# Kernel tuning notes

Measured on AMD Instinct MI355X. Metric: run time of the kernel, lower is better.

The kernel has to match this reference:

```python
import jax, jax.numpy as jnp
import numpy as np

EPS = 1e-5

def _layernorm(x, g, b):
    mu = jnp.mean(x, axis=-1, keepdims=True)
    var = jnp.var(x, axis=-1, keepdims=True)
    return (x - mu) * jax.lax.rsqrt(var + EPS) * g + b

def _pos_encoding(S, D, dtype):
    pos = jnp.arange(S, dtype=jnp.float32)[:, None]
    div = jnp.exp(jnp.arange(0, D, 2, dtype=jnp.float32) * (-jnp.log(10000.0) / D))
    pe = jnp.zeros((S, D), dtype=jnp.float32)
    pe = pe.at[:, 0::2].set(jnp.sin(pos * div))
    pe = pe.at[:, 1::2].set(jnp.cos(pos * div))
    return pe.astype(dtype)

def setup_inputs() -> dict:
    key = jax.random.key(0)
    B, S, D, H, F, L = 4, 1024, 768, 12, 3072, 6
    ks = jax.random.split(key, 8)
    s = 0.02
    return {
        "x": jax.random.normal(ks[0], (B, S, D), jnp.float32),
        "Wqkv": jax.random.normal(ks[1], (L, D, 3 * D), jnp.float32) * s,
        "bqkv": jnp.zeros((L, 3 * D), jnp.float32),
        "Wo": jax.random.normal(ks[2], (L, D, D), jnp.float32) * s,
        "bo": jnp.zeros((L, D), jnp.float32),
        "ln1_g": jnp.ones((L, D), jnp.float32),
        "ln1_b": jnp.zeros((L, D), jnp.float32),
        "W1": jax.random.normal(ks[3], (L, D, F), jnp.float32) * s,
        "b1": jnp.zeros((L, F), jnp.float32),
        "W2": jax.random.normal(ks[4], (L, F, D), jnp.float32) * s,
        "b2": jnp.zeros((L, D), jnp.float32),
        "ln2_g": jnp.ones((L, D), jnp.float32),
        "ln2_b": jnp.zeros((L, D), jnp.float32),
        "lnf_g": jnp.ones((D,), jnp.float32),
        "lnf_b": jnp.zeros((D,), jnp.float32),
        "num_heads": 12,
    }

def reference(x, Wqkv, bqkv, Wo, bo, ln1_g, ln1_b, W1, b1, W2, b2, ln2_g, ln2_b, lnf_g, lnf_b, num_heads):
    B, S, D = x.shape
    H = num_heads
    hd = D // H
    scale = 1.0 / jnp.sqrt(jnp.float32(hd)).astype(x.dtype)

    x = x + _pos_encoding(S, D, x.dtype)[None]

    def layer(h, params):
        wqkv, bq, wo, bo_, g1, b1_, w1, bias1, w2, bias2, g2, b2_ = params
        qkv = (h @ wqkv + bq).reshape(B, S, 3, H, hd)
        q, k, v = jnp.moveaxis(qkv, 2, 0)          # each [B,S,H,hd]
        q = q.transpose(0, 2, 1, 3)                 # bhqd
        k = k.transpose(0, 2, 1, 3)
        v = v.transpose(0, 2, 1, 3)
        scores = jnp.einsum('bhqd,bhkd->bhqk', q, k) * scale
        w = jax.nn.softmax(scores, axis=-1)
        w = jnp.clip(w, 1e-6, 1.0)                  # clamp as in torch module
        attn = jnp.einsum('bhqk,bhkd->bhqd', w, v)
        attn = attn.transpose(0, 2, 1, 3).reshape(B, S, D) @ wo + bo_
        h = _layernorm(h + attn, g1, b1_)
        ffn = jax.nn.relu(h @ w1 + bias1) @ w2 + bias2
        h = _layernorm(h + ffn, g2, b2_)
        return h, None

    params = (Wqkv, bqkv, Wo, bo, ln1_g, ln1_b, W1, b1, W2, b2, ln2_g, ln2_b)
    x, _ = jax.lax.scan(layer, x, params)
    return _layernorm(x, lnf_g, lnf_b)
```

## Files before the change

kernel.cpp:

```cpp
#include <hip/hip_runtime.h>
#include <math.h>

typedef float f32x4 __attribute__((ext_vector_type(4)));
typedef __bf16 bf16x8 __attribute__((ext_vector_type(8)));
typedef unsigned short u16x8 __attribute__((ext_vector_type(8)));

__device__ __forceinline__ unsigned short f2bf(float f) {
    union { float f; unsigned int u; } v; v.f = f;
    unsigned int r = v.u + 0x7FFFu + ((v.u >> 16) & 1u);
    return (unsigned short)(r >> 16);
}
__device__ __forceinline__ float bf2f(unsigned short u) {
    union { unsigned int u; float f; } v; v.u = ((unsigned int)u) << 16;
    return v.f;
}
__device__ __forceinline__ bf16x8 ld8(const unsigned short* p) {
    union { u16x8 u; bf16x8 b; } c;
    c.u = *(const u16x8*)p;
    return c.b;
}
__device__ __forceinline__ void gload_lds16(const unsigned short* g, unsigned short* l) {
    __builtin_amdgcn_global_load_lds(
        (const __attribute__((address_space(1))) unsigned int*)g,
        (__attribute__((address_space(3))) unsigned int*)l,
        16, 0, 0);
}
__device__ __forceinline__ int swz_off(int row, int quad) {
    return row * 32 + ((quad ^ ((row >> 1) & 3)) << 3);
}

__global__ __launch_bounds__(256)
void transpose_convert(const float* __restrict__ W, unsigned short* __restrict__ Wt,
                       int K, int N) {
    __shared__ float tile[32][33];
    int n0 = blockIdx.x * 32, k0 = blockIdx.y * 32;
    int tx = threadIdx.x & 31, ty = threadIdx.x >> 5;
#pragma unroll
    for (int i = 0; i < 4; ++i) {
        int k = ty + i * 8;
        tile[k][tx] = W[(size_t)(k0 + k) * N + n0 + tx];
    }
    __syncthreads();
#pragma unroll
    for (int i = 0; i < 4; ++i) {
        int n = ty + i * 8;
        Wt[(size_t)(n0 + n) * K + k0 + tx] = f2bf(tile[tx][n]);
    }
}

__global__ __launch_bounds__(256)
void posenc_k(const float* __restrict__ x, float* __restrict__ h,
              unsigned short* __restrict__ hb) {
    int idx = blockIdx.x * 256 + threadIdx.x;
    const int TOT = 4 * 1024 * 768;
    if (idx >= TOT) return;
    int d = idx % 768;
    int s = (idx / 768) % 1024;
    int i2 = d >> 1;
    float dv = expf(-(float)(2 * i2) * (9.210340371976184f / 768.0f));
    float ang = (float)s * dv;
    float pe = (d & 1) ? cosf(ang) : sinf(ang);
    float v = x[idx] + pe;
    h[idx] = v;
    hb[idx] = f2bf(v);
}

template<int RELU, int BIAS>
__global__ __launch_bounds__(256)
void gemm_k(const unsigned short* __restrict__ A, const unsigned short* __restrict__ Bt,
            const float* __restrict__ bias, unsigned short* __restrict__ Cb,
            int M, int N, int K, int Kc) {
    __shared__ unsigned short As[2][128 * 32];
    __shared__ unsigned short Bs[2][128 * 32];
    const int tid = threadIdx.x;
    const int lane = tid & 63, wave = tid >> 6;
    const int l15 = lane & 15, quad = lane >> 4;
    const int m0 = blockIdx.y * 128, n0 = blockIdx.x * 128;
    const int wr = (wave >> 1) * 64, wc = (wave & 1) * 64;
    const int kstart = blockIdx.z * Kc;
    unsigned short* Cbp = Cb + (size_t)blockIdx.z * M * N;

    const int r0 = wave * 32 + (lane >> 2);
    const int kc0 = lane & 3;

    auto stage = [&](int k0, int bi) {
#pragma unroll
        for (int j = 0; j < 2; ++j) {
            int r = r0 + j * 16;
            int kcl = kc0 ^ ((r >> 1) & 3);
            gload_lds16(A + (size_t)(m0 + r) * K + k0 + kcl * 8,
                        &As[bi][(wave * 32 + j * 16) * 32]);
            gload_lds16(Bt + (size_t)(n0 + r) * K + k0 + kcl * 8,
                        &Bs[bi][(wave * 32 + j * 16) * 32]);
        }
    };

    f32x4 acc[4][4];
#pragma unroll
    for (int i = 0; i < 4; ++i)
#pragma unroll
        for (int j = 0; j < 4; ++j) acc[i][j] = (f32x4){0.f, 0.f, 0.f, 0.f};

    stage(kstart, 0);
    const int nk = Kc / 32;
    for (int t = 0; t < nk; ++t) {
        __syncthreads();
        if (t + 1 < nk) stage(kstart + (t + 1) * 32, (t + 1) & 1);
        const unsigned short* Asb = As[t & 1];
        const unsigned short* Bsb = Bs[t & 1];
        bf16x8 af[4], bfr[4];
#pragma unroll
        for (int mt = 0; mt < 4; ++mt)
            af[mt] = ld8(&Asb[swz_off(wr + mt * 16 + l15, quad)]);
#pragma unroll
        for (int nt = 0; nt < 4; ++nt)
            bfr[nt] = ld8(&Bsb[swz_off(wc + nt * 16 + l15, quad)]);
#pragma unroll
        for (int mt = 0; mt < 4; ++mt)
#pragma unroll
            for (int nt = 0; nt < 4; ++nt)
                acc[mt][nt] = __builtin_amdgcn_mfma_f32_16x16x32_bf16(
                    af[mt], bfr[nt], acc[mt][nt], 0, 0, 0);
    }
#pragma unroll
    for (int mt = 0; mt < 4; ++mt)
#pragma unroll
        for (int nt = 0; nt < 4; ++nt)
#pragma unroll
            for (int r = 0; r < 4; ++r) {
                int row = m0 + wr + mt * 16 + quad * 4 + r;
                int col = n0 + wc + nt * 16 + l15;
                float v = acc[mt][nt][r];
                if (BIAS) v += bias[col];
                if (RELU) v = fmaxf(v, 0.f);
                Cbp[(size_t)row * N + col] = f2bf(v);
            }
}

__global__ __launch_bounds__(256)
void qksplit_k(const unsigned short* __restrict__ qkv, unsigned short* __restrict__ Q,
               unsigned short* __restrict__ Ko) {
    int o8 = blockIdx.x * 256 + threadIdx.x;
    const int NQ8 = 393216;
    int which = (o8 >= NQ8) ? 1 : 0;
    int oo = o8 - which * NQ8;
    int dg = (oo & 7) * 8;
    int s = (oo >> 3) & 1023;
    int bh = oo >> 13;
    int h = bh % 12, b = bh / 12;
    size_t row = (size_t)(b * 1024 + s);
    int col = which * 768 + h * 64 + dg;
    u16x8 val = *(const u16x8*)&qkv[row * 2304 + col];
    if (!which) {
#pragma unroll
        for (int j = 0; j < 8; ++j) val[j] = f2bf(bf2f(val[j]) * 0.125f);
        *(u16x8*)&Q[((size_t)bh * 1024 + s) * 64 + dg] = val;
    } else {
        *(u16x8*)&Ko[((size_t)bh * 1024 + s) * 64 + dg] = val;
    }
}

__global__ __launch_bounds__(256)
void vt_k(const unsigned short* __restrict__ qkv, unsigned short* __restrict__ Vt) {
    __shared__ unsigned short t[64][65];
    int bh = blockIdx.y, s0 = blockIdx.x * 64;
    int b = bh / 12, h = bh % 12;
    int tx = threadIdx.x & 63;
    int ty = threadIdx.x >> 6;
#pragma unroll
    for (int r = 0; r < 16; ++r) {
        int i = ty + r * 4;
        t[i][tx] = qkv[(size_t)(b * 1024 + s0 + i) * 2304 + 1536 + h * 64 + tx];
    }
    __syncthreads();
#pragma unroll
    for (int r = 0; r < 16; ++r) {
        int dd = ty + r * 4;
        Vt[((size_t)bh * 64 + dd) * 1024 + s0 + tx] = t[tx][dd];
    }
}

#define PSTR 68
__global__ __launch_bounds__(256)
void flash_k(const unsigned short* __restrict__ Q, const unsigned short* __restrict__ K,
             const unsigned short* __restrict__ Vt, unsigned short* __restrict__ ctx) {
    const int S = 1024, HD = 64;
    int bh = blockIdx.y;
    int b = bh / 12, h = bh % 12;
    int q0 = blockIdx.x * 64;
    const unsigned short* Qp = Q + ((size_t)bh * S + q0) * HD;
    const unsigned short* Kp = K + (size_t)bh * S * HD;
    const unsigned short* Vp = Vt + (size_t)bh * HD * S;

    __shared__ unsigned short Qs[128 * 32];
    __shared__ unsigned short Ks[2][128 * 32];
    __shared__ unsigned short Vs[2][128 * 32];
    __shared__ unsigned short Ps[4 * 16 * PSTR];

    int tid = threadIdx.x;
    int lane = tid & 63, wave = tid >> 6;
    int l15 = lane & 15, quad = lane >> 4;

    const int rl0 = lane >> 2;
    const int c0 = lane & 3;

    auto stageKV = [&](int kt, int bi) {
#pragma unroll
        for (int j = 0; j < 2; ++j) {
            int R = wave * 32 + j * 16 + rl0;
            int khalf = R >> 6, grow = R & 63;
            int lch = c0 ^ ((R >> 1) & 3);
            gload_lds16(Kp + (kt * 64 + grow) * HD + khalf * 32 + lch * 8,
                        &Ks[bi][(wave * 32 + j * 16) * 32]);
            gload_lds16(Vp + (size_t)grow * S + kt * 64 + khalf * 32 + lch * 8,
                        &Vs[bi][(wave * 32 + j * 16) * 32]);
        }
    };

#pragma unroll
    for (int j = 0; j < 2; ++j) {
        int R = wave * 32 + j * 16 + rl0;
        int khalf = R >> 6, grow = R & 63;
        int lch = c0 ^ ((R >> 1) & 3);
        gload_lds16(Qp + grow * HD + khalf * 32 + lch * 8,
                    &Qs[(wave * 32 + j * 16) * 32]);
    }
    stageKV(0, 0);

    f32x4 o[4];
#pragma unroll
    for (int i = 0; i < 4; ++i) o[i] = (f32x4){0.f, 0.f, 0.f, 0.f};
    float lsum[4] = {0.f, 0.f, 0.f, 0.f};

    unsigned short* Pw = &Ps[wave * 16 * PSTR];

    for (int kt = 0; kt < 16; ++kt) {
        __syncthreads();
        if (kt < 15) stageKV(kt + 1, (kt + 1) & 1);
        const unsigned short* Ksb = Ks[kt & 1];
        const unsigned short* Vsb = Vs[kt & 1];

        bf16x8 qa0 = ld8(&Qs[swz_off(wave * 16 + l15, quad)]);
        bf16x8 qa1 = ld8(&Qs[swz_off(64 + wave * 16 + l15, quad)]);
        f32x4 sc[4];
#pragma unroll
        for (int cb = 0; cb < 4; ++cb) {
            bf16x8 kb0 = ld8(&Ksb[swz_off(cb * 16 + l15, quad)]);
            bf16x8 kb1 = ld8(&Ksb[swz_off(64 + cb * 16 + l15, quad)]);
            f32x4 z = (f32x4){0.f, 0.f, 0.f, 0.f};
            z = __builtin_amdgcn_mfma_f32_16x16x32_bf16(qa0, kb0, z, 0, 0, 0);
            z = __builtin_amdgcn_mfma_f32_16x16x32_bf16(qa1, kb1, z, 0, 0, 0);
            sc[cb] = z;
        }
#pragma unroll
        for (int cb = 0; cb < 4; ++cb)
#pragma unroll
            for (int r = 0; r < 4; ++r) {
                float pv = __expf(sc[cb][r]);
                sc[cb][r] = pv;
                lsum[r] += pv;
            }
#pragma unroll
        for (int cb = 0; cb < 4; ++cb)
#pragma unroll
            for (int r = 0; r < 4; ++r)
                Pw[(quad * 4 + r) * PSTR + cb * 16 + l15] = f2bf(sc[cb][r]);
        bf16x8 pa0 = ld8(&Pw[l15 * PSTR + quad * 8]);
        bf16x8 pa1 = ld8(&Pw[l15 * PSTR + 32 + quad * 8]);
#pragma unroll
        for (int cb = 0; cb < 4; ++cb) {
            bf16x8 vb0 = ld8(&Vsb[swz_off(cb * 16 + l15, quad)]);
            bf16x8 vb1 = ld8(&Vsb[swz_off(64 + cb * 16 + l15, quad)]);
            o[cb] = __builtin_amdgcn_mfma_f32_16x16x32_bf16(pa0, vb0, o[cb], 0, 0, 0);
            o[cb] = __builtin_amdgcn_mfma_f32_16x16x32_bf16(pa1, vb1, o[cb], 0, 0, 0);
        }
    }
#pragma unroll
    for (int r = 0; r < 4; ++r) {
#pragma unroll
        for (int off = 1; off < 16; off <<= 1) lsum[r] += __shfl_xor(lsum[r], off);
    }
#pragma unroll
    for (int cb = 0; cb < 4; ++cb)
#pragma unroll
        for (int r = 0; r < 4; ++r) {
            int row = q0 + wave * 16 + quad * 4 + r;
            float val = o[cb][r] / lsum[r];
            ctx[((size_t)(b * 1024 + row)) * 768 + h * 64 + cb * 16 + l15] = f2bf(val);
        }
}

template<int NPART, int WBF16>
__global__ __launch_bounds__(256)
void ln_k(const float* __restrict__ X, const unsigned short* __restrict__ P,
          const float* __restrict__ pb,
          const float* __restrict__ g, const float* __restrict__ bta,
          float* __restrict__ Yf, unsigned short* __restrict__ Yb) {
    const int D = 768;
    const size_t MD = (size_t)4096 * 768;
    int row = blockIdx.x;
    int tid = threadIdx.x;
    const float* x = X + (size_t)row * D;
    float v[3];
    float s = 0.f, s2 = 0.f;
#pragma unroll
    for (int i = 0; i < 3; ++i) {
        int c = i * 256 + tid;
        float t = x[c];
        if (NPART > 0) {
            float r = pb[c];
#pragma unroll
            for (int pi = 0; pi < NPART; ++pi)
                r += bf2f(P[MD * pi + (size_t)row * D + c]);
            t += r;
        }
        v[i] = t;
        s += t;
        s2 += t * t;
    }
#pragma unroll
    for (int off = 1; off < 64; off <<= 1) {
        s += __shfl_xor(s, off);
        s2 += __shfl_xor(s2, off);
    }
    __shared__ float rs[4], rs2[4];
    int wave = tid >> 6, lane = tid & 63;
    if (lane == 0) { rs[wave] = s; rs2[wave] = s2; }
    __syncthreads();
    s = rs[0] + rs[1] + rs[2] + rs[3];
    s2 = rs2[0] + rs2[1] + rs2[2] + rs2[3];
    float mu = s * (1.f / 768.f);
    float var = s2 * (1.f / 768.f) - mu * mu;
    float rstd = rsqrtf(var + 1e-5f);
#pragma unroll
    for (int i = 0; i < 3; ++i) {
        int c = i * 256 + tid;
        float y = (v[i] - mu) * rstd * g[c] + bta[c];
        Yf[(size_t)row * D + c] = y;
        if (WBF16) Yb[(size_t)row * D + c] = f2bf(y);
    }
}

extern "C" void kernel_launch(void* const* d_in, const int* in_sizes, int n_in,
                              void* d_out, int out_size, void* d_ws, size_t ws_size,
                              hipStream_t stream) {
    const float* x    = (const float*)d_in[0];
    const float* Wqkv = (const float*)d_in[1];
    const float* bqkv = (const float*)d_in[2];
    const float* Wo   = (const float*)d_in[3];
    const float* bo   = (const float*)d_in[4];
    const float* ln1g = (const float*)d_in[5];
    const float* ln1b = (const float*)d_in[6];
    const float* W1   = (const float*)d_in[7];
    const float* b1   = (const float*)d_in[8];
    const float* W2   = (const float*)d_in[9];
    const float* b2   = (const float*)d_in[10];
    const float* ln2g = (const float*)d_in[11];
    const float* ln2b = (const float*)d_in[12];
    const float* lnfg = (const float*)d_in[13];
    const float* lnfb = (const float*)d_in[14];

    const int B = 4, S = 1024, D = 768, H = 12, F = 3072, L = 6;
    const int M = B * S;

    char* p = (char*)d_ws;
    auto alloc = [&](size_t bytes) -> char* {
        char* r = p;
        p += (bytes + 255) & ~(size_t)255;
        return r;
    };
    float* h             = (float*)alloc((size_t)M * D * 4);
    unsigned short* tmp  = (unsigned short*)alloc((size_t)4 * M * D * 2);
    unsigned short* hb   = (unsigned short*)alloc((size_t)M * D * 2);
    unsigned short* act  = (unsigned short*)alloc((size_t)M * F * 2);
    unsigned short* Qb   = (unsigned short*)alloc((size_t)M * D * 2);
    unsigned short* Kb   = (unsigned short*)alloc((size_t)M * D * 2);
    unsigned short* Vtb  = (unsigned short*)alloc((size_t)M * D * 2);
    unsigned short* ctx  = (unsigned short*)alloc((size_t)M * D * 2);
    unsigned short* wqkvT = (unsigned short*)alloc((size_t)3 * D * D * 2);
    unsigned short* woT   = (unsigned short*)alloc((size_t)D * D * 2);
    unsigned short* w1T   = (unsigned short*)alloc((size_t)D * F * 2);
    unsigned short* w2T   = (unsigned short*)alloc((size_t)D * F * 2);
    unsigned short* qkvb = act;
    unsigned short* f1b  = act;

    posenc_k<<<(M * D) / 256, 256, 0, stream>>>(x, h, hb);

    for (int l = 0; l < L; ++l) {
        transpose_convert<<<dim3(3 * D / 32, D / 32), 256, 0, stream>>>(
            Wqkv + (size_t)l * D * 3 * D, wqkvT, D, 3 * D);
        transpose_convert<<<dim3(D / 32, D / 32), 256, 0, stream>>>(
            Wo + (size_t)l * D * D, woT, D, D);
        transpose_convert<<<dim3(F / 32, D / 32), 256, 0, stream>>>(
            W1 + (size_t)l * D * F, w1T, D, F);
        transpose_convert<<<dim3(D / 32, F / 32), 256, 0, stream>>>(
            W2 + (size_t)l * F * D, w2T, F, D);

        gemm_k<0, 1><<<dim3(3 * D / 128, M / 128, 1), 256, 0, stream>>>(
            hb, wqkvT, bqkv + (size_t)l * 3 * D, qkvb, M, 3 * D, D, D);
        qksplit_k<<<786432 / 256, 256, 0, stream>>>(qkvb, Qb, Kb);
        vt_k<<<dim3(S / 64, B * H), 256, 0, stream>>>(qkvb, Vtb);
        flash_k<<<dim3(S / 64, B * H), 256, 0, stream>>>(Qb, Kb, Vtb, ctx);
        gemm_k<0, 0><<<dim3(D / 128, M / 128, 4), 256, 0, stream>>>(
            ctx, woT, nullptr, tmp, M, D, D, D / 4);
        ln_k<4, 1><<<M, 256, 0, stream>>>(h, tmp, bo + (size_t)l * D,
                                          ln1g + (size_t)l * D, ln1b + (size_t)l * D,
                                          h, hb);
        gemm_k<1, 1><<<dim3(F / 128, M / 128, 1), 256, 0, stream>>>(
            hb, w1T, b1 + (size_t)l * F, f1b, M, F, D, D);
        gemm_k<0, 0><<<dim3(D / 128, M / 128, 4), 256, 0, stream>>>(
            f1b, w2T, nullptr, tmp, M, D, F, F / 4);
        ln_k<4, 1><<<M, 256, 0, stream>>>(h, tmp, b2 + (size_t)l * D,
                                          ln2g + (size_t)l * D, ln2b + (size_t)l * D,
                                          h, hb);
    }
    ln_k<0, 0><<<M, 256, 0, stream>>>(h, nullptr, nullptr, lnfg, lnfb,
                                      (float*)d_out, nullptr);
}
```

Before: 1.319 ms.

## Split attention over key halves, fuse weight prep and QKV split kernels

Merges the four weight transpose-convert launches into one kernel, and merges the Q/K split and V transpose into one kernel. Q is now prescaled by 0.125·log2(e) so the softmax can use exp2. The flash kernel splits the key range across two z-blocks, single-buffers K/V to cut LDS use, computes row sums with an MFMA against a ones vector, and writes partial outputs that a new combine kernel adds and normalizes. This is meant to raise occupancy and parallelism in attention and reduce launch count. In exchange it costs an extra pass over the partial outputs, drops K/V prefetch overlap, and rounds P by truncation rather than round-to-nearest.

```diff
diff --git a/kernel.cpp b/kernel.cpp
--- a/kernel.cpp
+++ b/kernel.cpp
@@ -9,6 +9,10 @@
     union { float f; unsigned int u; } v; v.f = f;
     unsigned int r = v.u + 0x7FFFu + ((v.u >> 16) & 1u);
     return (unsigned short)(r >> 16);
+}
+__device__ __forceinline__ unsigned short f2bft(float f) {
+    union { float f; unsigned int u; } v; v.f = f;
+    return (unsigned short)(v.u >> 16);
 }
 __device__ __forceinline__ float bf2f(unsigned short u) {
     union { unsigned int u; float f; } v; v.u = ((unsigned int)u) << 16;
@@ -30,10 +34,19 @@
 }
 
 __global__ __launch_bounds__(256)
-void transpose_convert(const float* __restrict__ W, unsigned short* __restrict__ Wt,
-                       int K, int N) {
+void wprep_k(const float* __restrict__ Wqkv, const float* __restrict__ Wo,
+             const float* __restrict__ W1, const float* __restrict__ W2,
+             unsigned short* __restrict__ qkvT, unsigned short* __restrict__ woT,
+             unsigned short* __restrict__ w1T, unsigned short* __restrict__ w2T) {
     __shared__ float tile[32][33];
-    int n0 = blockIdx.x * 32, k0 = blockIdx.y * 32;
+    int bid = blockIdx.x;
+    const float* W; unsigned short* Wt; int K, N, idx;
+    if (bid < 1728)      { W = Wqkv; Wt = qkvT; K = 768;  N = 2304; idx = bid; }
+    else if (bid < 2304) { W = Wo;   Wt = woT;  K = 768;  N = 768;  idx = bid - 1728; }
+    else if (bid < 4608) { W = W1;   Wt = w1T;  K = 768;  N = 3072; idx = bid - 2304; }
+    else                 { W = W2;   Wt = w2T;  K = 3072; N = 768;  idx = bid - 4608; }
+    int ntile = N / 32;
+    int n0 = (idx % ntile) * 32, k0 = (idx / ntile) * 32;
     int tx = threadIdx.x & 31, ty = threadIdx.x >> 5;
 #pragma unroll
     for (int i = 0; i < 4; ++i) {
@@ -138,40 +151,31 @@
 }
 
 __global__ __launch_bounds__(256)
-void qksplit_k(const unsigned short* __restrict__ qkv, unsigned short* __restrict__ Q,
-               unsigned short* __restrict__ Ko) {
-    int o8 = blockIdx.x * 256 + threadIdx.x;
-    const int NQ8 = 393216;
-    int which = (o8 >= NQ8) ? 1 : 0;
-    int oo = o8 - which * NQ8;
-    int dg = (oo & 7) * 8;
-    int s = (oo >> 3) & 1023;
-    int bh = oo >> 13;
-    int h = bh % 12, b = bh / 12;
-    size_t row = (size_t)(b * 1024 + s);
-    int col = which * 768 + h * 64 + dg;
-    u16x8 val = *(const u16x8*)&qkv[row * 2304 + col];
-    if (!which) {
-#pragma unroll
-        for (int j = 0; j < 8; ++j) val[j] = f2bf(bf2f(val[j]) * 0.125f);
-        *(u16x8*)&Q[((size_t)bh * 1024 + s) * 64 + dg] = val;
-    } else {
-        *(u16x8*)&Ko[((size_t)bh * 1024 + s) * 64 + dg] = val;
-    }
-}
-
-__global__ __launch_bounds__(256)
-void vt_k(const unsigned short* __restrict__ qkv, unsigned short* __restrict__ Vt) {
+void qkv_prep(const unsigned short* __restrict__ qkv, unsigned short* __restrict__ Q,
+              unsigned short* __restrict__ Ko, unsigned short* __restrict__ Vt) {
     __shared__ unsigned short t[64][65];
     int bh = blockIdx.y, s0 = blockIdx.x * 64;
     int b = bh / 12, h = bh % 12;
-    int tx = threadIdx.x & 63;
-    int ty = threadIdx.x >> 6;
+    int tid = threadIdx.x;
+    int tx = tid & 63, ty = tid >> 6;
 #pragma unroll
     for (int r = 0; r < 16; ++r) {
         int i = ty + r * 4;
         t[i][tx] = qkv[(size_t)(b * 1024 + s0 + i) * 2304 + 1536 + h * 64 + tx];
     }
+    const float QS = 0.18033688088889765f;
+#pragma unroll
+    for (int it = 0; it < 2; ++it) {
+        int task = tid + it * 256;
+        int row = task >> 3, ch = (task & 7) * 8;
+        size_t src = (size_t)(b * 1024 + s0 + row) * 2304 + h * 64 + ch;
+        u16x8 qv = *(const u16x8*)&qkv[src];
+#pragma unroll
+        for (int j = 0; j < 8; ++j) qv[j] = f2bf(bf2f(qv[j]) * QS);
+        *(u16x8*)&Q[((size_t)bh * 1024 + s0 + row) * 64 + ch] = qv;
+        u16x8 kv = *(const u16x8*)&qkv[src + 768];
+        *(u16x8*)&Ko[((size_t)bh * 1024 + s0 + row) * 64 + ch] = kv;
+    }
     __syncthreads();
 #pragma unroll
     for (int r = 0; r < 16; ++r) {
@@ -180,42 +184,26 @@
     }
 }
 
-#define PSTR 68
 __global__ __launch_bounds__(256)
 void flash_k(const unsigned short* __restrict__ Q, const unsigned short* __restrict__ K,
-             const unsigned short* __restrict__ Vt, unsigned short* __restrict__ ctx) {
+             const unsigned short* __restrict__ Vt, unsigned short* __restrict__ O2,
+             float* __restrict__ ls) {
     const int S = 1024, HD = 64;
-    int bh = blockIdx.y;
-    int b = bh / 12, h = bh % 12;
+    int bh = blockIdx.y, b = bh / 12, h = bh % 12;
     int q0 = blockIdx.x * 64;
+    int zz = blockIdx.z;
     const unsigned short* Qp = Q + ((size_t)bh * S + q0) * HD;
     const unsigned short* Kp = K + (size_t)bh * S * HD;
     const unsigned short* Vp = Vt + (size_t)bh * HD * S;
 
-    __shared__ unsigned short Qs[128 * 32];
-    __shared__ unsigned short Ks[2][128 * 32];
-    __shared__ unsigned short Vs[2][128 * 32];
-    __shared__ unsigned short Ps[4 * 16 * PSTR];
-
-    int tid = threadIdx.x;
-    int lane = tid & 63, wave = tid >> 6;
+    __shared__ unsigned short sm[12288];
+    unsigned short* Qs = sm;
+    unsigned short* Ks = sm + 4096;
+    unsigned short* Vs = sm + 8192;
+
+    int tid = threadIdx.x, lane = tid & 63, wave = tid >> 6;
     int l15 = lane & 15, quad = lane >> 4;
-
-    const int rl0 = lane >> 2;
-    const int c0 = lane & 3;
-
-    auto stageKV = [&](int kt, int bi) {
-#pragma unroll
-        for (int j = 0; j < 2; ++j) {
-            int R = wave * 32 + j * 16 + rl0;
-            int khalf = R >> 6, grow = R & 63;
-            int lch = c0 ^ ((R >> 1) & 3);
-            gload_lds16(Kp + (kt * 64 + grow) * HD + khalf * 32 + lch * 8,
-                        &Ks[bi][(wave * 32 + j * 16) * 32]);
-            gload_lds16(Vp + (size_t)grow * S + kt * 64 + khalf * 32 + lch * 8,
-                        &Vs[bi][(wave * 32 + j * 16) * 32]);
-        }
-    };
+    const int rl0 = lane >> 2, c0 = lane & 3;
 
 #pragma unroll
     for (int j = 0; j < 2; ++j) {
@@ -225,28 +213,42 @@
         gload_lds16(Qp + grow * HD + khalf * 32 + lch * 8,
                     &Qs[(wave * 32 + j * 16) * 32]);
     }
-    stageKV(0, 0);
+    __syncthreads();
+    bf16x8 qa0 = ld8(&Qs[swz_off(wave * 16 + l15, quad)]);
+    bf16x8 qa1 = ld8(&Qs[swz_off(64 + wave * 16 + l15, quad)]);
 
     f32x4 o[4];
 #pragma unroll
     for (int i = 0; i < 4; ++i) o[i] = (f32x4){0.f, 0.f, 0.f, 0.f};
-    float lsum[4] = {0.f, 0.f, 0.f, 0.f};
-
-    unsigned short* Pw = &Ps[wave * 16 * PSTR];
-
-    for (int kt = 0; kt < 16; ++kt) {
+    f32x4 lacc = (f32x4){0.f, 0.f, 0.f, 0.f};
+    bf16x8 ones;
+    {
+        union { u16x8 u; bf16x8 b; } c;
+#pragma unroll
+        for (int j = 0; j < 8; ++j) c.u[j] = 0x3F80;
+        ones = c.b;
+    }
+    unsigned short* Pw = sm + wave * 1024;
+
+    for (int kt = zz * 8; kt < zz * 8 + 8; ++kt) {
         __syncthreads();
-        if (kt < 15) stageKV(kt + 1, (kt + 1) & 1);
-        const unsigned short* Ksb = Ks[kt & 1];
-        const unsigned short* Vsb = Vs[kt & 1];
-
-        bf16x8 qa0 = ld8(&Qs[swz_off(wave * 16 + l15, quad)]);
-        bf16x8 qa1 = ld8(&Qs[swz_off(64 + wave * 16 + l15, quad)]);
+#pragma unroll
+        for (int j = 0; j < 2; ++j) {
+            int R = wave * 32 + j * 16 + rl0;
+            int khalf = R >> 6, grow = R & 63;
+            int lch = c0 ^ ((R >> 1) & 3);
+            gload_lds16(Kp + (kt * 64 + grow) * HD + khalf * 32 + lch * 8,
+                        &Ks[(wave * 32 + j * 16) * 32]);
+            gload_lds16(Vp + (size_t)grow * S + kt * 64 + khalf * 32 + lch * 8,
+                        &Vs[(wave * 32 + j * 16) * 32]);
+        }
+        __syncthreads();
+
         f32x4 sc[4];
 #pragma unroll
         for (int cb = 0; cb < 4; ++cb) {
-            bf16x8 kb0 = ld8(&Ksb[swz_off(cb * 16 + l15, quad)]);
-            bf16x8 kb1 = ld8(&Ksb[swz_off(64 + cb * 16 + l15, quad)]);
+            bf16x8 kb0 = ld8(&Ks[swz_off(cb * 16 + l15, quad)]);
+            bf16x8 kb1 = ld8(&Ks[swz_off(64 + cb * 16 + l15, quad)]);
             f32x4 z = (f32x4){0.f, 0.f, 0.f, 0.f};
             z = __builtin_amdgcn_mfma_f32_16x16x32_bf16(qa0, kb0, z, 0, 0, 0);
             z = __builtin_amdgcn_mfma_f32_16x16x32_bf16(qa1, kb1, z, 0, 0, 0);
@@ -255,39 +257,55 @@
 #pragma unroll
         for (int cb = 0; cb < 4; ++cb)
 #pragma unroll
-            for (int r = 0; r < 4; ++r) {
-                float pv = __expf(sc[cb][r]);
-                sc[cb][r] = pv;
-                lsum[r] += pv;
-            }
-#pragma unroll
-        for (int cb = 0; cb < 4; ++cb)
-#pragma unroll
             for (int r = 0; r < 4; ++r)
-                Pw[(quad * 4 + r) * PSTR + cb * 16 + l15] = f2bf(sc[cb][r]);
-        bf16x8 pa0 = ld8(&Pw[l15 * PSTR + quad * 8]);
-        bf16x8 pa1 = ld8(&Pw[l15 * PSTR + 32 + quad * 8]);
+                Pw[(quad * 4 + r) * 64 + ((cb * 16 + l15) ^ (quad << 4))] =
+                    f2bft(__builtin_amdgcn_exp2f(sc[cb][r]));
+        bf16x8 pa0 = ld8(&Pw[l15 * 64 + ((quad * 8) ^ ((l15 >> 2) << 4))]);
+        bf16x8 pa1 = ld8(&Pw[l15 * 64 + ((32 + quad * 8) ^ ((l15 >> 2) << 4))]);
+        lacc = __builtin_amdgcn_mfma_f32_16x16x32_bf16(pa0, ones, lacc, 0, 0, 0);
+        lacc = __builtin_amdgcn_mfma_f32_16x16x32_bf16(pa1, ones, lacc, 0, 0, 0);
 #pragma unroll
         for (int cb = 0; cb < 4; ++cb) {
-            bf16x8 vb0 = ld8(&Vsb[swz_off(cb * 16 + l15, quad)]);
-            bf16x8 vb1 = ld8(&Vsb[swz_off(64 + cb * 16 + l15, quad)]);
+            bf16x8 vb0 = ld8(&Vs[swz_off(cb * 16 + l15, quad)]);
+            bf16x8 vb1 = ld8(&Vs[swz_off(64 + cb * 16 + l15, quad)]);
             o[cb] = __builtin_amdgcn_mfma_f32_16x16x32_bf16(pa0, vb0, o[cb], 0, 0, 0);
             o[cb] = __builtin_amdgcn_mfma_f32_16x16x32_bf16(pa1, vb1, o[cb], 0, 0, 0);
         }
     }
-#pragma unroll
-    for (int r = 0; r < 4; ++r) {
-#pragma unroll
-        for (int off = 1; off < 16; off <<= 1) lsum[r] += __shfl_xor(lsum[r], off);
-    }
+    unsigned short* Op = O2 + (size_t)zz * 4096 * 768;
 #pragma unroll
     for (int cb = 0; cb < 4; ++cb)
 #pragma unroll
         for (int r = 0; r < 4; ++r) {
             int row = q0 + wave * 16 + quad * 4 + r;
-            float val = o[cb][r] / lsum[r];
-            ctx[((size_t)(b * 1024 + row)) * 768 + h * 64 + cb * 16 + l15] = f2bf(val);
-        }
+            Op[((size_t)(b * 1024 + row)) * 768 + h * 64 + cb * 16 + l15] =
+                f2bf(o[cb][r]);
+        }
+    if (l15 == 0) {
+#pragma unroll
+        for (int r = 0; r < 4; ++r)
+            ls[zz * 49152 + bh * 1024 + q0 + wave * 16 + quad * 4 + r] = lacc[r];
+    }
+}
+
+__global__ __launch_bounds__(256)
+void attn_combine_k(const unsigned short* __restrict__ O2, const float* __restrict__ ls,
+                    unsigned short* __restrict__ ctx) {
+    int idx = blockIdx.x * 256 + threadIdx.x;
+    int ch = idx % 96;
+    int row = idx / 96;
+    int col = ch * 8;
+    int b = row >> 10, s = row & 1023, h = col >> 6;
+    const size_t MD = (size_t)4096 * 768;
+    u16x8 o0 = *(const u16x8*)&O2[(size_t)row * 768 + col];
+    u16x8 o1 = *(const u16x8*)&O2[MD + (size_t)row * 768 + col];
+    int li = (b * 12 + h) * 1024 + s;
+    float rl = 1.0f / (ls[li] + ls[49152 + li]);
+    u16x8 ov;
+#pragma unroll
+    for (int j = 0; j < 8; ++j)
+        ov[j] = f2bf((bf2f(o0[j]) + bf2f(o1[j])) * rl);
+    *(u16x8*)&ctx[(size_t)row * 768 + col] = ov;
 }
 
 template<int NPART, int WBF16>
@@ -371,6 +389,7 @@
     };
     float* h             = (float*)alloc((size_t)M * D * 4);
     unsigned short* tmp  = (unsigned short*)alloc((size_t)4 * M * D * 2);
+    float* lsbuf         = (float*)alloc((size_t)2 * 48 * 1024 * 4);
     unsigned short* hb   = (unsigned short*)alloc((size_t)M * D * 2);
     unsigned short* act  = (unsigned short*)alloc((size_t)M * F * 2);
     unsigned short* Qb   = (unsigned short*)alloc((size_t)M * D * 2);
@@ -387,20 +406,16 @@
     posenc_k<<<(M * D) / 256, 256, 0, stream>>>(x, h, hb);
 
     for (int l = 0; l < L; ++l) {
-        transpose_convert<<<dim3(3 * D / 32, D / 32), 256, 0, stream>>>(
-            Wqkv + (size_t)l * D * 3 * D, wqkvT, D, 3 * D);
-        transpose_convert<<<dim3(D / 32, D / 32), 256, 0, stream>>>(
-            Wo + (size_t)l * D * D, woT, D, D);
-        transpose_convert<<<dim3(F / 32, D / 32), 256, 0, stream>>>(
-            W1 + (size_t)l * D * F, w1T, D, F);
-        transpose_convert<<<dim3(D / 32, F / 32), 256, 0, stream>>>(
-            W2 + (size_t)l * F * D, w2T, F, D);
+        wprep_k<<<6912, 256, 0, stream>>>(
+            Wqkv + (size_t)l * D * 3 * D, Wo + (size_t)l * D * D,
+            W1 + (size_t)l * D * F, W2 + (size_t)l * F * D,
+            wqkvT, woT, w1T, w2T);
 
         gemm_k<0, 1><<<dim3(3 * D / 128, M / 128, 1), 256, 0, stream>>>(
             hb, wqkvT, bqkv + (size_t)l * 3 * D, qkvb, M, 3 * D, D, D);
-        qksplit_k<<<786432 / 256, 256, 0, stream>>>(qkvb, Qb, Kb);
-        vt_k<<<dim3(S / 64, B * H), 256, 0, stream>>>(qkvb, Vtb);
-        flash_k<<<dim3(S / 64, B * H), 256, 0, stream>>>(Qb, Kb, Vtb, ctx);
+        qkv_prep<<<dim3(S / 64, B * H), 256, 0, stream>>>(qkvb, Qb, Kb, Vtb);
+        flash_k<<<dim3(S / 64, B * H, 2), 256, 0, stream>>>(Qb, Kb, Vtb, tmp, lsbuf);
+        attn_combine_k<<<(M * 96) / 256, 256, 0, stream>>>(tmp, lsbuf, ctx);
         gemm_k<0, 0><<<dim3(D / 128, M / 128, 4), 256, 0, stream>>>(
             ctx, woT, nullptr, tmp, M, D, D, D / 4);
         ln_k<4, 1><<<M, 256, 0, stream>>>(h, tmp, bo + (size_t)l * D,
```

Result: faster. 1.222 ms (-7.4%).
